# Optimization experiments

Measured on AMD Instinct MI355X. Metric: run time of the kernel, lower is better.

Reference implementation:

```python
import jax, jax.numpy as jnp
import numpy as np

EMB_DIM = 128
WEIGHT_COL = 24

def setup_inputs() -> dict:
    key = jax.random.key(0)
    ks = jax.random.split(key, 9)
    B, S = 8, 4096
    s_in = 1.0 / np.sqrt(EMB_DIM)
    s_out = 1.0 / np.sqrt(WEIGHT_COL)
    return {
        "x": jax.random.normal(ks[0], (B, S, EMB_DIM), dtype=jnp.float32),
        "wQ": jax.random.uniform(ks[1], (EMB_DIM, WEIGHT_COL), jnp.float32, -s_in, s_in),
        "bQ": jax.random.uniform(ks[2], (WEIGHT_COL,), jnp.float32, -s_in, s_in),
        "wK": jax.random.uniform(ks[3], (EMB_DIM, WEIGHT_COL), jnp.float32, -s_in, s_in),
        "bK": jax.random.uniform(ks[4], (WEIGHT_COL,), jnp.float32, -s_in, s_in),
        "wV": jax.random.uniform(ks[5], (EMB_DIM, WEIGHT_COL), jnp.float32, -s_in, s_in),
        "bV": jax.random.uniform(ks[6], (WEIGHT_COL,), jnp.float32, -s_in, s_in),
        "wO": jax.random.uniform(ks[7], (WEIGHT_COL, EMB_DIM), jnp.float32, -s_out, s_out),
        "bO": jax.random.uniform(ks[8], (EMB_DIM,), jnp.float32, -s_out, s_out),
    }

def reference(x, wQ, bQ, wK, bK, wV, bV, wO, bO):
    # projections: [B,S,E] -> [B,S,D]
    Q = x @ wQ + bQ
    K = x @ wK + bK
    V = x @ wV + bV
    # NOTE: source scales by sqrt(emb_dim), not sqrt(weight_col)
    scale = 1.0 / np.sqrt(EMB_DIM).astype(np.float32)
    scores = jnp.einsum('bqd,bkd->bqk', Q, K) * scale  # [B,S,S]
    A = jax.nn.softmax(scores, axis=-1)
    H = jnp.einsum('bqk,bkd->bqd', A, V)               # [B,S,D]
    return H @ wO + bO                                  # [B,S,E]
```

## Files before the change

kernel.cpp:

```cpp
#include <hip/hip_runtime.h>
#include <hip/hip_fp16.h>


#define B_ 8
#define S_ 4096
#define E_ 128
#define D_ 24
#define N_ (B_ * S_)
#define SCALE 0.08838834764831845f
#define LOG2E 1.4426950408889634f

#define TK 128
#define KS_STRIDE 40
#define VS_STRIDE 136
#define HS_STRIDE 40
#define XS_STRIDE 136
#define OS_STRIDE 84

typedef __attribute__((ext_vector_type(8))) short bfrag;
typedef __attribute__((ext_vector_type(4))) float ffrag;

__device__ inline unsigned short f2bf(float f) {
    unsigned int x = __builtin_bit_cast(unsigned int, f);
    return (unsigned short)((x + 0x7fffu + ((x >> 16) & 1u)) >> 16);
}
__device__ inline unsigned int pack2h(float a, float b) {
    unsigned int ua = __builtin_bit_cast(unsigned int, a) + 0x8000u;
    unsigned int ub = __builtin_bit_cast(unsigned int, b) + 0x8000u;
    return __builtin_amdgcn_perm(ub, ua, 0x07060302);
}
__device__ inline unsigned int packh16(float a, float b) {
    return __builtin_bit_cast(unsigned int, __builtin_amdgcn_cvt_pkrtz(a, b));
}

__global__ __launch_bounds__(256) void prep_kernel(
    const float* __restrict__ wQ, const float* __restrict__ bQ,
    const float* __restrict__ wK, const float* __restrict__ bK,
    const float* __restrict__ wV, const float* __restrict__ bV,
    const float* __restrict__ wO,
    unsigned short* __restrict__ Wf, unsigned short* __restrict__ wOf,
    float* __restrict__ bqkv)
{
    const int gtid   = blockIdx.x * 256 + threadIdx.x;
    const int stride = gridDim.x * 256;
    const float qs = SCALE * LOG2E;
    for (int idx = gtid; idx < 4 * 5 * 512; idx += stride) {
        const int j    = idx & 7;
        const int lane = (idx >> 3) & 63;
        const int nt   = (idx >> 9) % 5;
        const int kt   = idx / 2560;
        const int n = nt * 16 + (lane & 15);
        const int k = kt * 32 + ((lane >> 4) << 3) + j;
        float v = 0.0f;
        if (n < 24)      v = wQ[k * 24 + n] * qs;
        else if (n < 48) v = wK[k * 24 + (n - 24)];
        else if (n < 72) v = wV[k * 24 + (n - 48)];
        Wf[idx] = f2bf(v);
    }
    for (int idx = gtid; idx < 8 * 512; idx += stride) {
        const int j    = idx & 7;
        const int lane = (idx >> 3) & 63;
        const int nt   = idx >> 9;
        const int k = ((lane >> 4) << 3) + j;
        const int e = nt * 16 + (lane & 15);
        wOf[idx] = (k < 24) ? f2bf(wO[k * 128 + e]) : (unsigned short)0;
    }
    if (gtid < 80) {
        float v = 0.0f;
        if (gtid < 24)      v = bQ[gtid] * qs;
        else if (gtid < 48) v = bK[gtid - 24];
        else if (gtid < 72) v = bV[gtid - 48];
        bqkv[gtid] = v;
    }
}

__global__ __launch_bounds__(256) void proj_kernel(
    const float* __restrict__ x, const unsigned short* __restrict__ Wf,
    const float* __restrict__ bqkv,
    unsigned short* __restrict__ Qbf, unsigned short* __restrict__ Kbf,
    unsigned short* __restrict__ Vt)
{
    __shared__ float smem[64 * OS_STRIDE];
    unsigned short* xs = (unsigned short*)smem;
    float* os = smem;

    const int tid  = threadIdx.x;
    const int lane = tid & 63;
    const int w    = tid >> 6;
    const int col  = lane & 15;
    const int quad = lane >> 4;
    const int rb   = blockIdx.x * 64;

    #pragma unroll
    for (int i = 0; i < 8; ++i) {
        const int idx = i * 256 + tid;
        const int row = idx >> 5, c4 = idx & 31;
        const float4 xv = *(const float4*)(x + (size_t)(rb + row) * 128 + c4 * 4);
        uint2 h;
        h.x = pack2h(xv.x, xv.y);
        h.y = pack2h(xv.z, xv.w);
        *(uint2*)(&xs[row * XS_STRIDE + c4 * 4]) = h;
    }

    bfrag Wfr[20];
    #pragma unroll
    for (int f = 0; f < 20; ++f)
        Wfr[f] = *(const bfrag*)(Wf + (f * 64 + lane) * 8);

    __syncthreads();

    ffrag acc[5];
    #pragma unroll
    for (int nt = 0; nt < 5; ++nt) acc[nt] = (ffrag){0.f, 0.f, 0.f, 0.f};

    #pragma unroll
    for (int kt = 0; kt < 4; ++kt) {
        const bfrag Af = *(const bfrag*)(&xs[(w * 16 + col) * XS_STRIDE + kt * 32 + quad * 8]);
        #pragma unroll
        for (int nt = 0; nt < 5; ++nt)
            acc[nt] = __builtin_amdgcn_mfma_f32_16x16x32_bf16(Af, Wfr[kt * 5 + nt], acc[nt], 0, 0, 0);
    }

    __syncthreads();

    #pragma unroll
    for (int nt = 0; nt < 5; ++nt) {
        const float bb = bqkv[nt * 16 + col];
        #pragma unroll
        for (int r = 0; r < 4; ++r)
            os[(w * 16 + quad * 4 + r) * OS_STRIDE + nt * 16 + col] = acc[nt][r] + bb;
    }
    __syncthreads();

    {
        const int half  = tid & 1;
        const int row   = (tid >> 1) & 63;
        const int isK   = tid >> 7;
        const int cbase = isK * 24;
        unsigned int pk[8];
        #pragma unroll
        for (int g = 0; g < 8; ++g) {
            const int c0 = half * 16 + g * 2;
            const float f0 = (c0     < 24) ? os[row * OS_STRIDE + cbase + c0]     : 0.0f;
            const float f1 = (c0 + 1 < 24) ? os[row * OS_STRIDE + cbase + c0 + 1] : 0.0f;
            pk[g] = pack2h(f0, f1);
        }
        unsigned short* dst = (isK ? Kbf : Qbf) + (size_t)(rb + row) * 32 + half * 16;
        *(uint4*)(dst)     = make_uint4(pk[0], pk[1], pk[2], pk[3]);
        *(uint4*)(dst + 8) = make_uint4(pk[4], pk[5], pk[6], pk[7]);
    }

    if (tid < 192) {
        const int d  = tid % 24;
        const int ch = tid / 24;
        unsigned int p[4];
        #pragma unroll
        for (int g = 0; g < 4; ++g) {
            const float f0 = os[(ch * 8 + g * 2 + 0) * OS_STRIDE + 48 + d];
            const float f1 = os[(ch * 8 + g * 2 + 1) * OS_STRIDE + 48 + d];
            p[g] = pack2h(f0, f1);
        }
        const int b = rb >> 12, s0 = rb & 4095;
        uint4* dst = (uint4*)(Vt + (((size_t)(b * 24 + d)) << 12) + s0 + ch * 8);
        *dst = make_uint4(p[0], p[1], p[2], p[3]);
    }
}

__global__ __launch_bounds__(512, 8) void attn_kernel(
    const unsigned short* __restrict__ Qbf, const unsigned short* __restrict__ Kbf,
    const unsigned short* __restrict__ Vt,
    __half* __restrict__ Opart, float* __restrict__ lpart)
{
    __shared__ unsigned short Ks[TK * KS_STRIDE];
    __shared__ unsigned short Vs[32 * VS_STRIDE];

    const int tid    = threadIdx.x;
    const int lane   = tid & 63;
    const int w      = tid >> 6;
    const int col    = lane & 15;
    const int quad   = lane >> 4;
    const int blk    = blockIdx.x;
    const int split  = blockIdx.y;
    const int nsp    = gridDim.y;
    const int kchunk = S_ / nsp;
    const int b      = blk >> 5;
    const int qbase  = blk * 128 + w * 16;

    if (tid < 16)
        *(uint4*)(&Vs[24 * VS_STRIDE + tid * 8]) =
            make_uint4(0x3F803F80u, 0x3F803F80u, 0x3F803F80u, 0x3F803F80u);

    const bfrag Qf = *(const bfrag*)(Qbf + (size_t)(qbase + col) * 32 + quad * 8);

    ffrag Ot0 = {0.f, 0.f, 0.f, 0.f};
    ffrag Ot1 = {0.f, 0.f, 0.f, 0.f};

    const unsigned short* Kbase = Kbf + ((size_t)(b * 4096) + split * kchunk) * 32;
    const unsigned short* Vbase = Vt + (size_t)(b * 24) * 4096 + split * kchunk;

    __syncthreads();

    for (int kb = 0; kb < kchunk; kb += TK) {
        {
            const int key = tid >> 2, ch = tid & 3;
            const uint4 t4 = *(const uint4*)(Kbase + (size_t)(kb + key) * 32 + ch * 8);
            const int row = (key & ~31) + (((key >> 2) & 1) << 4)
                          + (((key & 31) >> 3) << 2) + (key & 3);
            *(uint4*)(&Ks[row * KS_STRIDE + ch * 8]) = t4;
        }
        if (tid < 384) {
            const int d = tid >> 4, ch = tid & 15;
            const uint4 t4 = *(const uint4*)(Vbase + (size_t)d * 4096 + kb + ch * 8);
            *(uint4*)(&Vs[d * VS_STRIDE + ch * 8]) = t4;
        }
        __syncthreads();

        #pragma unroll
        for (int c2 = 0; c2 < 4; ++c2) {
            const bfrag Kfe = *(const bfrag*)(&Ks[(c2 * 32 + col) * KS_STRIDE + quad * 8]);
            const bfrag Kfo = *(const bfrag*)(&Ks[(c2 * 32 + 16 + col) * KS_STRIDE + quad * 8]);
            ffrag Se = {0.f, 0.f, 0.f, 0.f};
            ffrag So = {0.f, 0.f, 0.f, 0.f};
            Se = __builtin_amdgcn_mfma_f32_16x16x32_bf16(Kfe, Qf, Se, 0, 0, 0);
            So = __builtin_amdgcn_mfma_f32_16x16x32_bf16(Kfo, Qf, So, 0, 0, 0);
            union { bfrag f; unsigned int u[4]; } P;
            P.u[0] = pack2h(__builtin_amdgcn_exp2f(Se[0]), __builtin_amdgcn_exp2f(Se[1]));
            P.u[1] = pack2h(__builtin_amdgcn_exp2f(Se[2]), __builtin_amdgcn_exp2f(Se[3]));
            P.u[2] = pack2h(__builtin_amdgcn_exp2f(So[0]), __builtin_amdgcn_exp2f(So[1]));
            P.u[3] = pack2h(__builtin_amdgcn_exp2f(So[2]), __builtin_amdgcn_exp2f(So[3]));
            const bfrag Va0 = *(const bfrag*)(&Vs[col * VS_STRIDE + c2 * 32 + quad * 8]);
            const bfrag Va1 = *(const bfrag*)(&Vs[(16 + col) * VS_STRIDE + c2 * 32 + quad * 8]);
            Ot0 = __builtin_amdgcn_mfma_f32_16x16x32_bf16(Va0, P.f, Ot0, 0, 0, 0);
            Ot1 = __builtin_amdgcn_mfma_f32_16x16x32_bf16(Va1, P.f, Ot1, 0, 0, 0);
        }
        __syncthreads();
    }

    const size_t base = ((size_t)split * N_ + qbase + col) * 32;
    {
        uint2 s0;
        s0.x = packh16(Ot0[0], Ot0[1]);
        s0.y = packh16(Ot0[2], Ot0[3]);
        *(uint2*)(Opart + base + quad * 4) = s0;
    }
    if (quad < 2) {
        uint2 s1;
        s1.x = packh16(Ot1[0], Ot1[1]);
        s1.y = packh16(Ot1[2], Ot1[3]);
        *(uint2*)(Opart + base + 16 + quad * 4) = s1;
    }
    if (quad == 2)
        lpart[(size_t)split * N_ + qbase + col] = Ot1[0];
}

__global__ __launch_bounds__(256) void combine_kernel(
    const __half* __restrict__ Opart, const float* __restrict__ lpart,
    const unsigned short* __restrict__ wOf, const float* __restrict__ bO,
    float* __restrict__ out, int nsp)
{
    __shared__ unsigned short Hs[64 * HS_STRIDE];

    const int tid = threadIdx.x;
    const int qb  = blockIdx.x * 64;
    {
        const int ql = tid >> 2;
        const int c8 = (tid & 3) * 8;
        const int q  = qb + ql;
        float a[8] = {0.f, 0.f, 0.f, 0.f, 0.f, 0.f, 0.f, 0.f};
        if (c8 < 24) {
            for (int s = 0; s < nsp; ++s) {
                const __half2* p2 = (const __half2*)(Opart + ((size_t)s * N_ + q) * 32 + c8);
                #pragma unroll
                for (int j = 0; j < 4; ++j) {
                    const float2 f = __half22float2(p2[j]);
                    a[2 * j]     += f.x;
                    a[2 * j + 1] += f.y;
                }
            }
        }
        float ls = 0.f;
        for (int s = 0; s < nsp; ++s) ls += lpart[(size_t)s * N_ + q];
        const float inv = 1.0f / ls;
        uint4 pk;
        pk.x = pack2h(a[0] * inv, a[1] * inv);
        pk.y = pack2h(a[2] * inv, a[3] * inv);
        pk.z = pack2h(a[4] * inv, a[5] * inv);
        pk.w = pack2h(a[6] * inv, a[7] * inv);
        *(uint4*)(&Hs[ql * HS_STRIDE + c8]) = pk;
    }
    __syncthreads();

    const int lane = tid & 63;
    const int w    = tid >> 6;
    const int col  = lane & 15;
    const int quad = lane >> 4;
    const bfrag Hf = *(const bfrag*)(&Hs[(w * 16 + col) * HS_STRIDE + quad * 8]);
    #pragma unroll
    for (int nt = 0; nt < 8; ++nt) {
        const bfrag Wo = *(const bfrag*)(wOf + (nt * 64 + lane) * 8);
        ffrag C = {0.f, 0.f, 0.f, 0.f};
        C = __builtin_amdgcn_mfma_f32_16x16x32_bf16(Hf, Wo, C, 0, 0, 0);
        const float bo = bO[nt * 16 + col];
        #pragma unroll
        for (int r = 0; r < 4; ++r)
            out[(size_t)(qb + w * 16 + quad * 4 + r) * 128 + nt * 16 + col] = C[r] + bo;
    }
}

extern "C" void kernel_launch(void* const* d_in, const int* in_sizes, int n_in,
                              void* d_out, int out_size, void* d_ws, size_t ws_size,
                              hipStream_t stream) {
    const float* x  = (const float*)d_in[0];
    const float* wQ = (const float*)d_in[1];
    const float* bQ = (const float*)d_in[2];
    const float* wK = (const float*)d_in[3];
    const float* bK = (const float*)d_in[4];
    const float* wV = (const float*)d_in[5];
    const float* bV = (const float*)d_in[6];
    const float* wO = (const float*)d_in[7];
    const float* bO = (const float*)d_in[8];
    float* out = (float*)d_out;

    unsigned short* ws16 = (unsigned short*)d_ws;
    unsigned short* Qbf = ws16;
    unsigned short* Kbf = Qbf + (size_t)N_ * 32;
    unsigned short* Vt  = Kbf + (size_t)N_ * 32;
    unsigned short* Wf  = Vt + (size_t)B_ * 24 * S_;
    unsigned short* wOf = Wf + 4 * 5 * 512;
    float* bqkv = (float*)(wOf + 8 * 512);
    __half* Opart = (__half*)(bqkv + 80);
    const size_t baseBytes = (size_t)((char*)Opart - (char*)d_ws);

    int nsp = 4;
    while (nsp > 1) {
        const size_t need = baseBytes + (size_t)nsp * N_ * 32 * 2 + (size_t)nsp * N_ * 4;
        if (need <= ws_size) break;
        nsp >>= 1;
    }
    float* lpart = (float*)(Opart + (size_t)nsp * N_ * 32);

    prep_kernel<<<8, 256, 0, stream>>>(wQ, bQ, wK, bK, wV, bV, wO, Wf, wOf, bqkv);
    proj_kernel<<<N_ / 64, 256, 0, stream>>>(x, Wf, bqkv, Qbf, Kbf, Vt);
    attn_kernel<<<dim3(N_ / 128, nsp), 512, 0, stream>>>(Qbf, Kbf, Vt, Opart, lpart);
    combine_kernel<<<N_ / 64, 256, 0, stream>>>(Opart, lpart, wOf, bO, out, nsp);
}
```

Measured before the change: 122.3 us.

## Switch attention to 32x32x16 MFMA tiles with 256-query blocks and more splits

Rewrites the attention inner loop to use 32x32x16 bf16 MFMA instead of 16x16x32. Each wave now handles 32 queries and each block 256, so every K/V tile loaded into LDS feeds twice as many queries. The K-row permutation in LDS and the output write-back are remapped to the 32x32 accumulator layout. To keep enough blocks in flight with half as many query blocks, the key-split count rises from 4 to 8 and the occupancy hint drops. The larger accumulators raise register pressure, and the extra splits add partial-result traffic and combine work.

After: 128.1 us. 4.7% more time.

```diff
diff --git a/kernel.cpp b/kernel.cpp
--- a/kernel.cpp
+++ b/kernel.cpp
@@ -19,6 +19,7 @@
 
 typedef __attribute__((ext_vector_type(8))) short bfrag;
 typedef __attribute__((ext_vector_type(4))) float ffrag;
+typedef __attribute__((ext_vector_type(16))) float ffrag16;
 
 __device__ inline unsigned short f2bf(float f) {
     unsigned int x = __builtin_bit_cast(unsigned int, f);
@@ -166,7 +167,7 @@
     }
 }
 
-__global__ __launch_bounds__(512, 8) void attn_kernel(
+__global__ __launch_bounds__(512, 4) void attn_kernel(
     const unsigned short* __restrict__ Qbf, const unsigned short* __restrict__ Kbf,
     const unsigned short* __restrict__ Vt,
     __half* __restrict__ Opart, float* __restrict__ lpart)
@@ -177,23 +178,23 @@
     const int tid    = threadIdx.x;
     const int lane   = tid & 63;
     const int w      = tid >> 6;
-    const int col    = lane & 15;
-    const int quad   = lane >> 4;
+    const int q32    = lane & 31;
+    const int h      = lane >> 5;
     const int blk    = blockIdx.x;
     const int split  = blockIdx.y;
     const int nsp    = gridDim.y;
     const int kchunk = S_ / nsp;
-    const int b      = blk >> 5;
-    const int qbase  = blk * 128 + w * 16;
+    const int b      = blk >> 4;
+    const int qbase  = blk * 256 + w * 32;
 
     if (tid < 16)
         *(uint4*)(&Vs[24 * VS_STRIDE + tid * 8]) =
             make_uint4(0x3F803F80u, 0x3F803F80u, 0x3F803F80u, 0x3F803F80u);
 
-    const bfrag Qf = *(const bfrag*)(Qbf + (size_t)(qbase + col) * 32 + quad * 8);
-
-    ffrag Ot0 = {0.f, 0.f, 0.f, 0.f};
-    ffrag Ot1 = {0.f, 0.f, 0.f, 0.f};
+    const bfrag Qf0 = *(const bfrag*)(Qbf + (size_t)(qbase + q32) * 32 + h * 8);
+    const bfrag Qf1 = *(const bfrag*)(Qbf + (size_t)(qbase + q32) * 32 + 16 + h * 8);
+
+    ffrag16 O = {0.f,0.f,0.f,0.f,0.f,0.f,0.f,0.f,0.f,0.f,0.f,0.f,0.f,0.f,0.f,0.f};
 
     const unsigned short* Kbase = Kbf + ((size_t)(b * 4096) + split * kchunk) * 32;
     const unsigned short* Vbase = Vt + (size_t)(b * 24) * 4096 + split * kchunk;
@@ -204,8 +205,8 @@
         {
             const int key = tid >> 2, ch = tid & 3;
             const uint4 t4 = *(const uint4*)(Kbase + (size_t)(kb + key) * 32 + ch * 8);
-            const int row = (key & ~31) + (((key >> 2) & 1) << 4)
-                          + (((key & 31) >> 3) << 2) + (key & 3);
+            const int kl  = key & 31;
+            const int row = (key & ~31) | (kl & 19) | ((kl & 4) << 1) | ((kl & 8) >> 1);
             *(uint4*)(&Ks[row * KS_STRIDE + ch * 8]) = t4;
         }
         if (tid < 384) {
@@ -216,41 +217,40 @@
         __syncthreads();
 
         #pragma unroll
-        for (int c2 = 0; c2 < 4; ++c2) {
-            const bfrag Kfe = *(const bfrag*)(&Ks[(c2 * 32 + col) * KS_STRIDE + quad * 8]);
-            const bfrag Kfo = *(const bfrag*)(&Ks[(c2 * 32 + 16 + col) * KS_STRIDE + quad * 8]);
-            ffrag Se = {0.f, 0.f, 0.f, 0.f};
-            ffrag So = {0.f, 0.f, 0.f, 0.f};
-            Se = __builtin_amdgcn_mfma_f32_16x16x32_bf16(Kfe, Qf, Se, 0, 0, 0);
-            So = __builtin_amdgcn_mfma_f32_16x16x32_bf16(Kfo, Qf, So, 0, 0, 0);
-            union { bfrag f; unsigned int u[4]; } P;
-            P.u[0] = pack2h(__builtin_amdgcn_exp2f(Se[0]), __builtin_amdgcn_exp2f(Se[1]));
-            P.u[1] = pack2h(__builtin_amdgcn_exp2f(Se[2]), __builtin_amdgcn_exp2f(Se[3]));
-            P.u[2] = pack2h(__builtin_amdgcn_exp2f(So[0]), __builtin_amdgcn_exp2f(So[1]));
-            P.u[3] = pack2h(__builtin_amdgcn_exp2f(So[2]), __builtin_amdgcn_exp2f(So[3]));
-            const bfrag Va0 = *(const bfrag*)(&Vs[col * VS_STRIDE + c2 * 32 + quad * 8]);
-            const bfrag Va1 = *(const bfrag*)(&Vs[(16 + col) * VS_STRIDE + c2 * 32 + quad * 8]);
-            Ot0 = __builtin_amdgcn_mfma_f32_16x16x32_bf16(Va0, P.f, Ot0, 0, 0, 0);
-            Ot1 = __builtin_amdgcn_mfma_f32_16x16x32_bf16(Va1, P.f, Ot1, 0, 0, 0);
+        for (int g = 0; g < 4; ++g) {
+            const bfrag Kf0 = *(const bfrag*)(&Ks[(g * 32 + q32) * KS_STRIDE + h * 8]);
+            const bfrag Kf1 = *(const bfrag*)(&Ks[(g * 32 + q32) * KS_STRIDE + 16 + h * 8]);
+            ffrag16 S = {0.f,0.f,0.f,0.f,0.f,0.f,0.f,0.f,0.f,0.f,0.f,0.f,0.f,0.f,0.f,0.f};
+            S = __builtin_amdgcn_mfma_f32_32x32x16_bf16(Kf0, Qf0, S, 0, 0, 0);
+            S = __builtin_amdgcn_mfma_f32_32x32x16_bf16(Kf1, Qf1, S, 0, 0, 0);
+            union { bfrag f; unsigned int u[4]; } P1, P2;
+            P1.u[0] = pack2h(__builtin_amdgcn_exp2f(S[0]),  __builtin_amdgcn_exp2f(S[1]));
+            P1.u[1] = pack2h(__builtin_amdgcn_exp2f(S[2]),  __builtin_amdgcn_exp2f(S[3]));
+            P1.u[2] = pack2h(__builtin_amdgcn_exp2f(S[4]),  __builtin_amdgcn_exp2f(S[5]));
+            P1.u[3] = pack2h(__builtin_amdgcn_exp2f(S[6]),  __builtin_amdgcn_exp2f(S[7]));
+            P2.u[0] = pack2h(__builtin_amdgcn_exp2f(S[8]),  __builtin_amdgcn_exp2f(S[9]));
+            P2.u[1] = pack2h(__builtin_amdgcn_exp2f(S[10]), __builtin_amdgcn_exp2f(S[11]));
+            P2.u[2] = pack2h(__builtin_amdgcn_exp2f(S[12]), __builtin_amdgcn_exp2f(S[13]));
+            P2.u[3] = pack2h(__builtin_amdgcn_exp2f(S[14]), __builtin_amdgcn_exp2f(S[15]));
+            const bfrag Va0 = *(const bfrag*)(&Vs[q32 * VS_STRIDE + g * 32 + h * 8]);
+            const bfrag Va1 = *(const bfrag*)(&Vs[q32 * VS_STRIDE + g * 32 + 16 + h * 8]);
+            O = __builtin_amdgcn_mfma_f32_32x32x16_bf16(Va0, P1.f, O, 0, 0, 0);
+            O = __builtin_amdgcn_mfma_f32_32x32x16_bf16(Va1, P2.f, O, 0, 0, 0);
         }
         __syncthreads();
     }
 
-    const size_t base = ((size_t)split * N_ + qbase + col) * 32;
-    {
-        uint2 s0;
-        s0.x = packh16(Ot0[0], Ot0[1]);
-        s0.y = packh16(Ot0[2], Ot0[3]);
-        *(uint2*)(Opart + base + quad * 4) = s0;
-    }
-    if (quad < 2) {
-        uint2 s1;
-        s1.x = packh16(Ot1[0], Ot1[1]);
-        s1.y = packh16(Ot1[2], Ot1[3]);
-        *(uint2*)(Opart + base + 16 + quad * 4) = s1;
-    }
-    if (quad == 2)
-        lpart[(size_t)split * N_ + qbase + col] = Ot1[0];
+    const size_t base = ((size_t)split * N_ + qbase + q32) * 32;
+    if (h == 0) {
+        *(uint2*)(Opart + base +  0) = make_uint2(packh16(O[0], O[1]),  packh16(O[2],  O[3]));
+        *(uint2*)(Opart + base +  8) = make_uint2(packh16(O[4], O[5]),  packh16(O[6],  O[7]));
+        *(uint2*)(Opart + base + 16) = make_uint2(packh16(O[8], O[9]),  packh16(O[10], O[11]));
+        lpart[(size_t)split * N_ + qbase + q32] = O[12];
+    } else {
+        *(uint2*)(Opart + base +  4) = make_uint2(packh16(O[0], O[1]),  packh16(O[2],  O[3]));
+        *(uint2*)(Opart + base + 12) = make_uint2(packh16(O[4], O[5]),  packh16(O[6],  O[7]));
+        *(uint2*)(Opart + base + 20) = make_uint2(packh16(O[8], O[9]),  packh16(O[10], O[11]));
+    }
 }
 
 __global__ __launch_bounds__(256) void combine_kernel(
@@ -331,7 +331,7 @@
     __half* Opart = (__half*)(bqkv + 80);
     const size_t baseBytes = (size_t)((char*)Opart - (char*)d_ws);
 
-    int nsp = 4;
+    int nsp = 8;
     while (nsp > 1) {
         const size_t need = baseBytes + (size_t)nsp * N_ * 32 * 2 + (size_t)nsp * N_ * 4;
         if (need <= ws_size) break;
@@ -341,6 +341,6 @@
 
     prep_kernel<<<8, 256, 0, stream>>>(wQ, bQ, wK, bK, wV, bV, wO, Wf, wOf, bqkv);
     proj_kernel<<<N_ / 64, 256, 0, stream>>>(x, Wf, bqkv, Qbf, Kbf, Vt);
-    attn_kernel<<<dim3(N_ / 128, nsp), 512, 0, stream>>>(Qbf, Kbf, Vt, Opart, lpart);
+    attn_kernel<<<dim3(N_ / 256, nsp), 512, 0, stream>>>(Qbf, Kbf, Vt, Opart, lpart);
     combine_kernel<<<N_ / 64, 256, 0, stream>>>(Opart, lpart, wOf, bO, out, nsp);
 }
```
